# Optimization experiments

Measured on AMD Instinct MI355X. Metric: run time of the kernel, lower is better.

Reference implementation:

```python
import jax, jax.numpy as jnp
import numpy as np

B, T, C, H = 4, 2048, 1024, 16
HD = C // H  # head dim = 64

def setup_inputs() -> dict:
    key = jax.random.key(0)
    k1, k2, k3 = jax.random.split(key, 3)
    x = jax.random.normal(k1, (B, T, C), dtype=jnp.float32)
    w_attn = jax.random.normal(k2, (C, 3 * C), dtype=jnp.float32) * 0.02
    w_proj = jax.random.normal(k3, (C, C), dtype=jnp.float32) * 0.02
    return {"x": x, "w_attn": w_attn, "w_proj": w_proj}

def reference(x, w_attn, w_proj):
    b, t, c = x.shape
    qkv = x @ w_attn  # [B,T,3C]
    q, k, v = jnp.split(qkv, 3, axis=-1)
    # [B,T,C] -> [B,H,T,HD]
    def heads(z):
        return z.reshape(b, t, H, HD).transpose(0, 2, 1, 3)
    q, k, v = heads(q), heads(k), heads(v)
    scale = 1.0 / jnp.sqrt(jnp.float32(HD))
    att = jnp.einsum('bhqd,bhkd->bhqk', q, k) * scale  # [B,H,T,T]
    causal = jnp.tril(jnp.ones((t, t), dtype=bool))
    att = jnp.where(causal[None, None], att, -jnp.inf)
    att = jax.nn.softmax(att, axis=-1)
    y = jnp.einsum('bhqk,bhkd->bhqd', att, v)  # [B,H,T,HD]
    y = y.transpose(0, 2, 1, 3).reshape(b, t, c)
    return y @ w_proj
```

## Files before the change

### kernel.cpp

```cpp
#include <hip/hip_runtime.h>
#include <hip/hip_bf16.h>

typedef short bf16x8 __attribute__((ext_vector_type(8)));
typedef short short4v __attribute__((ext_vector_type(4)));
typedef float f32x4 __attribute__((ext_vector_type(4)));

template <bool V> struct BoolC { static constexpr bool value = V; };

__device__ __forceinline__ short f2b(float f) {
  __hip_bfloat16 h = __float2bfloat16(f);
  union { __hip_bfloat16 h; short s; } u; u.h = h; return u.s;
}

__device__ __forceinline__ void async_copy16(const short* g, short* l) {
  __builtin_amdgcn_global_load_lds((const __attribute__((address_space(1))) void*)g,
                                   (__attribute__((address_space(3))) void*)l, 16, 0, 0);
}

__global__ __launch_bounds__(256) void pre_kernel(const float* __restrict__ x, short* __restrict__ xb,
                                                  const float* __restrict__ wa, short* __restrict__ waT,
                                                  const float* __restrict__ wp, short* __restrict__ wpT,
                                                  float qscale) {
  const int tid = threadIdx.x;
  const int blk = blockIdx.x;
  if (blk < 8192) {
    const int i = blk * 256 + tid;
    const float4 v = ((const float4*)x)[i];
    short4v o;
    o[0] = f2b(v.x); o[1] = f2b(v.y); o[2] = f2b(v.z); o[3] = f2b(v.w);
    ((short4v*)xb)[i] = o;
    return;
  }
  __shared__ float t[32][33];
  const float* in; short* out;
  int idx, gxb, Cn, qrows; float qs;
  if (blk < 11264) { idx = blk - 8192;  in = wa; out = waT; gxb = 96; Cn = 3072; qrows = 1024; qs = qscale; }
  else             { idx = blk - 11264; in = wp; out = wpT; gxb = 32; Cn = 1024; qrows = 0;    qs = 1.0f; }
  const int bx = idx % gxb, by = idx / gxb;
  const int tx = tid & 31, ty = tid >> 5;
  const int c0 = bx * 32, r0 = by * 32;
#pragma unroll
  for (int yy = 0; yy < 32; yy += 8)
    t[ty + yy][tx] = in[(size_t)(r0 + ty + yy) * Cn + (c0 + tx)];
  __syncthreads();
#pragma unroll
  for (int yy = 0; yy < 32; yy += 8) {
    const int orow = c0 + ty + yy;
    float v = t[tx][ty + yy];
    if (orow < qrows) v *= qs;
    out[(size_t)orow * 1024 + (r0 + tx)] = f2b(v);
  }
}

__global__ __launch_bounds__(256) void vtrans_kernel(const short* __restrict__ qkv,
                                                     short* __restrict__ vT) {
  constexpr int T = 2048, C3 = 3072, HD = 64;
  const int bh = blockIdx.y, b = bh >> 4, h = bh & 15;
  const int t0 = blockIdx.x * 64;
  __shared__ short tile[64][72];
  const int tid = threadIdx.x;
  const int tr = tid >> 2, dc = (tid & 3) * 16;
  const short* src = qkv + (size_t)b * T * C3 + (size_t)(t0 + tr) * C3 + 2048 + h * HD + dc;
  *(bf16x8*)&tile[tr][dc] = *(const bf16x8*)src;
  *(bf16x8*)&tile[tr][dc + 8] = *(const bf16x8*)(src + 8);
  __syncthreads();
  const int dr = tid >> 2, tc = (tid & 3) * 16;
  bf16x8 o0, o1;
#pragma unroll
  for (int i = 0; i < 8; i++) o0[i] = tile[tc + i][dr];
#pragma unroll
  for (int i = 0; i < 8; i++) o1[i] = tile[tc + 8 + i][dr];
  short* dst = vT + ((size_t)bh * HD + dr) * T + t0 + tc;
  *(bf16x8*)dst = o0;
  *(bf16x8*)(dst + 8) = o1;
}

template <int BN, typename OutT>
__global__ __launch_bounds__(512, 2) void gemm8p_kernel(const short* __restrict__ A,
                                                        const short* __restrict__ Bt,
                                                        OutT* __restrict__ C,
                                                        int M, int N, int K) {
  constexpr int NB = BN / 64;
  constexpr int NSTREAM = NB + 4;
  __shared__ short ldsA[2][16384];
  __shared__ short ldsB[2][NB * 4096];

  const int tid = threadIdx.x;
  const int w = tid >> 6, lane = tid & 63;
  const int quad = lane >> 4, l16 = lane & 15;
  const int half = w >> 2;
  const int wn = (w & 3) * (BN / 4);
  const int wm = half * 128;

  const int gx = gridDim.x;
  const int nwg = gx * gridDim.y;
  const int flat = blockIdx.y * gx + blockIdx.x;
  const int swz = (flat & 7) * (nwg >> 3) + (flat >> 3);
  const int bn = swz % gx, bm = swz / gx;
  const int m0 = bm * 256, n0 = bn * BN;

  const int rsub = lane >> 3;
  const int cl = (lane & 7) ^ rsub;
  const short* pAsrc = A + (size_t)(m0 + half * 128 + (w & 3) * 8 + rsub) * K + cl * 8;
  const short* pBsrc = Bt + (size_t)(n0 + w * 8 + rsub) * K + cl * 8;
  const int dstoff = w * 512;

  f32x4 acc[8][NB] = {};
  bf16x8 bfr[NB][2];

  auto issue = [&](int i, int buf, int tt) {
    if (i < NB)
      async_copy16(pBsrc + (size_t)(i * 64) * K + tt * 64, &ldsB[buf][i * 4096 + dstoff]);
    else
      async_copy16(pAsrc + (size_t)((i - NB) * 32) * K + tt * 64,
                   &ldsA[buf][(i - NB) * 4096 + dstoff]);
  };

#pragma unroll
  for (int i = 0; i < NSTREAM; ++i) issue(i, 0, 0);

  const int NT = K >> 6;

#define GEMM_PHASE(P, GS, GL)                                                                  \
  {                                                                                            \
    if constexpr (LAST) { asm volatile("s_waitcnt vmcnt(" #GL ")" ::: "memory"); }             \
    else                { asm volatile("s_waitcnt vmcnt(" #GS ")" ::: "memory"); }             \
    __builtin_amdgcn_s_barrier();                                                              \
    asm volatile("" ::: "memory");                                                             \
    bf16x8 af[2][2];                                                                           \
    _Pragma("unroll") for (int mm = 0; mm < 2; ++mm)                                           \
    _Pragma("unroll") for (int kh = 0; kh < 2; ++kh)                                           \
      af[mm][kh] = *(const bf16x8*)&ldsA[buf][((P * 2 + half) * 32 + mm * 16 + l16) * 64 +     \
                                              (((kh * 4 + quad) ^ (l16 & 7)) * 8)];            \
    if constexpr (P == 0) {                                                                    \
      _Pragma("unroll") for (int nf = 0; nf < NB; ++nf)                                        \
      _Pragma("unroll") for (int kh = 0; kh < 2; ++kh)                                         \
        bfr[nf][kh] = *(const bf16x8*)&ldsB[buf][(wn + nf * 16 + l16) * 64 +                   \
                                                 (((kh * 4 + quad) ^ (l16 & 7)) * 8)];         \
    }                                                                                          \
    if constexpr (!LAST) {                                                                     \
      if constexpr (2 * P < NSTREAM) issue(2 * P, buf ^ 1, t + 1);                             \
      if constexpr (2 * P + 1 < NSTREAM) issue(2 * P + 1, buf ^ 1, t + 1);                     \
    }                                                                                          \
    __builtin_amdgcn_s_setprio(1);                                                             \
    _Pragma("unroll") for (int mm = 0; mm < 2; ++mm)                                           \
    _Pragma("unroll") for (int nf = 0; nf < NB; ++nf) {                                        \
      acc[P * 2 + mm][nf] = __builtin_amdgcn_mfma_f32_16x16x32_bf16(af[mm][0], bfr[nf][0],     \
                                                                    acc[P * 2 + mm][nf], 0, 0, 0); \
      acc[P * 2 + mm][nf] = __builtin_amdgcn_mfma_f32_16x16x32_bf16(af[mm][1], bfr[nf][1],     \
                                                                    acc[P * 2 + mm][nf], 0, 0, 0); \
    }                                                                                          \
    __builtin_amdgcn_s_setprio(0);                                                             \
    __builtin_amdgcn_s_barrier();                                                              \
  }

  auto tile = [&](int t, auto lastc) {
    constexpr bool LAST = decltype(lastc)::value;
    const int buf = t & 1;
    GEMM_PHASE(0, 3, 3)
    GEMM_PHASE(1, 4, 2)
    GEMM_PHASE(2, 5, 1)
    GEMM_PHASE(3, 6, 0)
  };

  for (int t = 0; t < NT - 1; ++t) tile(t, BoolC<false>{});
  tile(NT - 1, BoolC<true>{});
#undef GEMM_PHASE

  (void)M;
#pragma unroll
  for (int mf = 0; mf < 8; ++mf)
#pragma unroll
    for (int nf = 0; nf < NB; ++nf) {
      const int col = n0 + wn + nf * 16 + l16;
#pragma unroll
      for (int r = 0; r < 4; ++r) {
        const int row = m0 + wm + mf * 16 + quad * 4 + r;
        if constexpr (sizeof(OutT) == 4)
          C[(size_t)row * N + col] = acc[mf][nf][r];
        else
          C[(size_t)row * N + col] = f2b(acc[mf][nf][r]);
      }
    }
}

__global__ __launch_bounds__(256, 2) void attn_kernel(const short* __restrict__ qkv,
                                                      const short* __restrict__ vT,
                                                      short* __restrict__ y) {
  constexpr int T = 2048, C3 = 3072, Cc = 1024, HD = 64;
  const int bh = blockIdx.y, b = bh >> 4, h = bh & 15;
  const int tid = threadIdx.x, lane = tid & 63, wave = tid >> 6;
  const int quad = lane >> 4, l16 = lane & 15;

  __shared__ short Ksb[2][64 * 64];
  __shared__ short Vtb[2][64 * 64];
  __shared__ short Ps[4][2][16 * 68];

  const size_t base = (size_t)b * T * C3;
  const int qcol = h * HD, kcol = Cc + h * HD;
  const size_t vtbase = (size_t)bh * HD * T;

  const int r8 = lane >> 3;
  const int cg8 = ((lane & 7) ^ r8) * 8;
  const short* gk[2];
  const short* gv[2];
  short* lk[2][2]; short* lv[2][2];
#pragma unroll
  for (int t8 = 0; t8 < 2; t8++) {
    const int row = wave * 16 + t8 * 8 + r8;
    gk[t8] = qkv + base + (size_t)row * C3 + kcol + cg8;
    gv[t8] = vT + vtbase + (size_t)row * T + cg8;
#pragma unroll
    for (int bu = 0; bu < 2; bu++) {
      lk[bu][t8] = &Ksb[bu][(wave * 16 + t8 * 8) * 64];
      lv[bu][t8] = &Vtb[bu][(wave * 16 + t8 * 8) * 64];
    }
  }
  const int sw0 = ((quad) ^ (l16 & 7)) * 8;
  const int sw1 = ((quad + 4) ^ (l16 & 7)) * 8;

  bf16x8 ones;
#pragma unroll
  for (int i = 0; i < 8; i++) ones[i] = (short)0x3F80;

  for (int half = 0; half < 2; half++) {
    const int t = half ? blockIdx.x : (15 - blockIdx.x);
    const int q0 = t * 128;
    const int jmax = 2 * t + 1;

    bf16x8 qf[2][2];
#pragma unroll
    for (int s = 0; s < 2; s++) {
      const short* qp = qkv + base + (size_t)(q0 + s * 64 + wave * 16 + l16) * C3 + qcol + quad * 8;
      qf[s][0] = *(const bf16x8*)qp;
      qf[s][1] = *(const bf16x8*)(qp + 32);
    }

    f32x4 o[2][4] = {};
    f32x4 l[2] = {};

    async_copy16(gk[0], lk[0][0]);
    async_copy16(gk[1], lk[0][1]);
    async_copy16(gv[0], lv[0][0]);
    async_copy16(gv[1], lv[0][1]);

    for (int j = 0; j <= jmax; j++) {
      const int cur = j & 1;
      __syncthreads();

      if (j < jmax) {
        const size_t ko = (size_t)(j + 1) * 64 * C3;
        const int vo = (j + 1) * 64;
        async_copy16(gk[0] + ko, lk[cur ^ 1][0]);
        async_copy16(gk[1] + ko, lk[cur ^ 1][1]);
        async_copy16(gv[0] + vo, lv[cur ^ 1][0]);
        async_copy16(gv[1] + vo, lv[cur ^ 1][1]);
      }

      bf16x8 kf[4][2], vf[4][2];
#pragma unroll
      for (int nt = 0; nt < 4; nt++) {
        const int rowb = (nt * 16 + l16) * 64;
        kf[nt][0] = *(const bf16x8*)&Ksb[cur][rowb + sw0];
        kf[nt][1] = *(const bf16x8*)&Ksb[cur][rowb + sw1];
        vf[nt][0] = *(const bf16x8*)&Vtb[cur][rowb + sw0];
        vf[nt][1] = *(const bf16x8*)&Vtb[cur][rowb + sw1];
      }

      const bool lo_act = (j < jmax);

#pragma unroll
      for (int s = 0; s < 2; s++) {
        if (s == 0 && !lo_act) continue;
        f32x4 sc[4];
#pragma unroll
        for (int nt = 0; nt < 4; nt++) {
          f32x4 a = {};
          a = __builtin_amdgcn_mfma_f32_16x16x32_bf16(qf[s][0], kf[nt][0], a, 0, 0, 0);
          a = __builtin_amdgcn_mfma_f32_16x16x32_bf16(qf[s][1], kf[nt][1], a, 0, 0, 0);
          sc[nt] = a;
        }
        const bool diag = (s == 0) ? (j == jmax - 1) : (j == jmax);
        if (diag) {
#pragma unroll
          for (int nt = 0; nt < 4; nt++)
#pragma unroll
            for (int r = 0; r < 4; r++) {
              const int row_l = wave * 16 + quad * 4 + r;
              const int col_l = nt * 16 + l16;
              if (col_l > row_l) sc[nt][r] = -INFINITY;
            }
        }
#pragma unroll
        for (int nt = 0; nt < 4; nt++)
#pragma unroll
          for (int r = 0; r < 4; r++)
            Ps[wave][s][(quad * 4 + r) * 68 + nt * 16 + l16] =
                f2b(__builtin_amdgcn_exp2f(sc[nt][r]));
      }
      asm volatile("s_waitcnt lgkmcnt(0)" ::: "memory");

#pragma unroll
      for (int s = 0; s < 2; s++) {
        if (s == 0 && !lo_act) continue;
        bf16x8 pa0 = *(const bf16x8*)&Ps[wave][s][l16 * 68 + quad * 8];
        bf16x8 pa1 = *(const bf16x8*)&Ps[wave][s][l16 * 68 + 32 + quad * 8];
        f32x4 lsum = {};
        lsum = __builtin_amdgcn_mfma_f32_16x16x32_bf16(pa0, ones, lsum, 0, 0, 0);
        lsum = __builtin_amdgcn_mfma_f32_16x16x32_bf16(pa1, ones, lsum, 0, 0, 0);
        l[s] += lsum;
#pragma unroll
        for (int nt = 0; nt < 4; nt++) {
          o[s][nt] = __builtin_amdgcn_mfma_f32_16x16x32_bf16(pa0, vf[nt][0], o[s][nt], 0, 0, 0);
          o[s][nt] = __builtin_amdgcn_mfma_f32_16x16x32_bf16(pa1, vf[nt][1], o[s][nt], 0, 0, 0);
        }
      }
    }

#pragma unroll
    for (int s = 0; s < 2; s++)
#pragma unroll
      for (int nt = 0; nt < 4; nt++)
#pragma unroll
        for (int r = 0; r < 4; r++) {
          const int row_g = q0 + s * 64 + wave * 16 + quad * 4 + r;
          y[(size_t)(b * T + row_g) * Cc + h * HD + nt * 16 + l16] = f2b(o[s][nt][r] / l[s][r]);
        }
  }
}

extern "C" void kernel_launch(void* const* d_in, const int* in_sizes, int n_in,
                              void* d_out, int out_size, void* d_ws, size_t ws_size,
                              hipStream_t stream) {
  constexpr int B = 4, T = 2048, C = 1024;
  constexpr int M = B * T;
  constexpr int N1 = 3 * C;
  const float* x      = (const float*)d_in[0];
  const float* w_attn = (const float*)d_in[1];
  const float* w_proj = (const float*)d_in[2];
  float* out = (float*)d_out;

  char* ws = (char*)d_ws;
  short* xb   = (short*)(ws + 0);
  short* waT  = (short*)(ws + 16777216);
  short* wpT  = (short*)(ws + 23068672);
  short* qkvb = (short*)(ws + 25165824);
  short* yb   = (short*)(ws + 75497472);
  short* vT   = xb;

  const float qscale = 0.125f * 1.44269504088896340736f;

  pre_kernel<<<12288, 256, 0, stream>>>(x, xb, w_attn, waT, w_proj, wpT, qscale);
  gemm8p_kernel<192, short><<<dim3(N1 / 192, M / 256), 512, 0, stream>>>(xb, waT, qkvb, M, N1, C);
  vtrans_kernel<<<dim3(T / 64, B * 16), 256, 0, stream>>>(qkvb, vT);
  attn_kernel<<<dim3(8, B * 16), 256, 0, stream>>>(qkvb, vT, yb);
  gemm8p_kernel<128, float><<<dim3(C / 128, M / 256), 512, 0, stream>>>(yb, wpT, out, M, C, C);
}
```

Before: 251.1 us.

## Switch attention to 32x32 MFMA with register-resident P and remapped block order

The attention kernel moves from 16x16x32 MFMAs to 32x32x16 MFMAs, with each wave owning 32 query rows. It computes S^T so the probabilities can be repacked in registers using cvt_pk_bf16 and permlane32_swap, which removes the LDS round trip for P and its waitcnt. Waves skip key tiles past their own causal diagonal and skip the upper 32-key half when it is fully masked. The change also adds s_setprio around MFMA bursts and remaps block indices so consecutive blocks spread across heads. The risks are higher register pressure from 16-wide accumulators and extra divergence in control flow between waves.

```diff
diff --git a/kernel.cpp b/kernel.cpp
--- a/kernel.cpp
+++ b/kernel.cpp
@@ -4,12 +4,23 @@
 typedef short bf16x8 __attribute__((ext_vector_type(8)));
 typedef short short4v __attribute__((ext_vector_type(4)));
 typedef float f32x4 __attribute__((ext_vector_type(4)));
+typedef float f32x16 __attribute__((ext_vector_type(16)));
 
 template <bool V> struct BoolC { static constexpr bool value = V; };
 
 __device__ __forceinline__ short f2b(float f) {
   __hip_bfloat16 h = __float2bfloat16(f);
   union { __hip_bfloat16 h; short s; } u; u.h = h; return u.s;
+}
+
+__device__ __forceinline__ unsigned cvtpk_bf16(float lo, float hi) {
+  unsigned r;
+  asm("v_cvt_pk_bf16_f32 %0, %1, %2" : "=v"(r) : "v"(lo), "v"(hi));
+  return r;
+}
+
+__device__ __forceinline__ f32x16 mfma32(bf16x8 a, bf16x8 b, f32x16 c) {
+  return __builtin_amdgcn_mfma_f32_32x32x16_bf16(a, b, c, 0, 0, 0);
 }
 
 __device__ __forceinline__ void async_copy16(const short* g, short* l) {
@@ -188,13 +199,15 @@
                                                       const short* __restrict__ vT,
                                                       short* __restrict__ y) {
   constexpr int T = 2048, C3 = 3072, Cc = 1024, HD = 64;
-  const int bh = blockIdx.y, b = bh >> 4, h = bh & 15;
+  const int f = blockIdx.y * 8 + blockIdx.x;
+  const int bh = (f & 7) * 8 + ((f >> 3) & 7);
+  const int xb = f >> 6;
+  const int b = bh >> 4, h = bh & 15;
   const int tid = threadIdx.x, lane = tid & 63, wave = tid >> 6;
-  const int quad = lane >> 4, l16 = lane & 15;
+  const int l32 = lane & 31, hi = lane >> 5;
 
   __shared__ short Ksb[2][64 * 64];
   __shared__ short Vtb[2][64 * 64];
-  __shared__ short Ps[4][2][16 * 68];
 
   const size_t base = (size_t)b * T * C3;
   const int qcol = h * HD, kcol = Cc + h * HD;
@@ -216,28 +229,27 @@
       lv[bu][t8] = &Vtb[bu][(wave * 16 + t8 * 8) * 64];
     }
   }
-  const int sw0 = ((quad) ^ (l16 & 7)) * 8;
-  const int sw1 = ((quad + 4) ^ (l16 & 7)) * 8;
+  const int rs7 = l32 & 7;
 
   bf16x8 ones;
 #pragma unroll
   for (int i = 0; i < 8; i++) ones[i] = (short)0x3F80;
 
   for (int half = 0; half < 2; half++) {
-    const int t = half ? blockIdx.x : (15 - blockIdx.x);
+    const int t = half ? xb : (15 - xb);
     const int q0 = t * 128;
     const int jmax = 2 * t + 1;
-
-    bf16x8 qf[2][2];
-#pragma unroll
-    for (int s = 0; s < 2; s++) {
-      const short* qp = qkv + base + (size_t)(q0 + s * 64 + wave * 16 + l16) * C3 + qcol + quad * 8;
-      qf[s][0] = *(const bf16x8*)qp;
-      qf[s][1] = *(const bf16x8*)(qp + 32);
+    const int jd = 2 * t + (wave >> 1);
+    const int qrow = q0 + wave * 32 + l32;
+
+    bf16x8 qf[4];
+    {
+      const short* qp = qkv + base + (size_t)qrow * C3 + qcol + hi * 8;
+#pragma unroll
+      for (int wk = 0; wk < 4; wk++) qf[wk] = *(const bf16x8*)(qp + wk * 16);
     }
 
-    f32x4 o[2][4] = {};
-    f32x4 l[2] = {};
+    f32x16 o0 = {}, o1 = {}, lC = {};
 
     async_copy16(gk[0], lk[0][0]);
     async_copy16(gk[1], lk[0][1]);
@@ -257,75 +269,108 @@
         async_copy16(gv[1] + vo, lv[cur ^ 1][1]);
       }
 
-      bf16x8 kf[4][2], vf[4][2];
-#pragma unroll
-      for (int nt = 0; nt < 4; nt++) {
-        const int rowb = (nt * 16 + l16) * 64;
-        kf[nt][0] = *(const bf16x8*)&Ksb[cur][rowb + sw0];
-        kf[nt][1] = *(const bf16x8*)&Ksb[cur][rowb + sw1];
-        vf[nt][0] = *(const bf16x8*)&Vtb[cur][rowb + sw0];
-        vf[nt][1] = *(const bf16x8*)&Vtb[cur][rowb + sw1];
-      }
-
-      const bool lo_act = (j < jmax);
-
-#pragma unroll
-      for (int s = 0; s < 2; s++) {
-        if (s == 0 && !lo_act) continue;
-        f32x4 sc[4];
-#pragma unroll
-        for (int nt = 0; nt < 4; nt++) {
-          f32x4 a = {};
-          a = __builtin_amdgcn_mfma_f32_16x16x32_bf16(qf[s][0], kf[nt][0], a, 0, 0, 0);
-          a = __builtin_amdgcn_mfma_f32_16x16x32_bf16(qf[s][1], kf[nt][1], a, 0, 0, 0);
-          sc[nt] = a;
+      if (j > jd) continue;
+
+      const bool up = (64 * j + 32) <= (q0 + wave * 32 + 31);
+
+      f32x16 st0 = {}, st1 = {};
+      __builtin_amdgcn_s_setprio(1);
+#pragma unroll
+      for (int wk = 0; wk < 4; wk++) {
+        const bf16x8 k0 = *(const bf16x8*)&Ksb[cur][l32 * 64 + (((2 * wk + hi) ^ rs7) * 8)];
+        st0 = mfma32(k0, qf[wk], st0);
+      }
+      if (up) {
+#pragma unroll
+        for (int wk = 0; wk < 4; wk++) {
+          const bf16x8 k1 = *(const bf16x8*)&Ksb[cur][(32 + l32) * 64 + (((2 * wk + hi) ^ rs7) * 8)];
+          st1 = mfma32(k1, qf[wk], st1);
         }
-        const bool diag = (s == 0) ? (j == jmax - 1) : (j == jmax);
-        if (diag) {
-#pragma unroll
-          for (int nt = 0; nt < 4; nt++)
-#pragma unroll
-            for (int r = 0; r < 4; r++) {
-              const int row_l = wave * 16 + quad * 4 + r;
-              const int col_l = nt * 16 + l16;
-              if (col_l > row_l) sc[nt][r] = -INFINITY;
-            }
+      }
+      __builtin_amdgcn_s_setprio(0);
+
+      if (j == jd) {
+#pragma unroll
+        for (int r = 0; r < 16; r++) {
+          const int kvl = 64 * j + (r & 3) + 8 * (r >> 2) + 4 * hi;
+          if (kvl > qrow) st0[r] = -INFINITY;
+          if (up && (kvl + 32 > qrow)) st1[r] = -INFINITY;
         }
-#pragma unroll
-        for (int nt = 0; nt < 4; nt++)
-#pragma unroll
-          for (int r = 0; r < 4; r++)
-            Ps[wave][s][(quad * 4 + r) * 68 + nt * 16 + l16] =
-                f2b(__builtin_amdgcn_exp2f(sc[nt][r]));
-      }
-      asm volatile("s_waitcnt lgkmcnt(0)" ::: "memory");
-
-#pragma unroll
-      for (int s = 0; s < 2; s++) {
-        if (s == 0 && !lo_act) continue;
-        bf16x8 pa0 = *(const bf16x8*)&Ps[wave][s][l16 * 68 + quad * 8];
-        bf16x8 pa1 = *(const bf16x8*)&Ps[wave][s][l16 * 68 + 32 + quad * 8];
-        f32x4 lsum = {};
-        lsum = __builtin_amdgcn_mfma_f32_16x16x32_bf16(pa0, ones, lsum, 0, 0, 0);
-        lsum = __builtin_amdgcn_mfma_f32_16x16x32_bf16(pa1, ones, lsum, 0, 0, 0);
-        l[s] += lsum;
-#pragma unroll
-        for (int nt = 0; nt < 4; nt++) {
-          o[s][nt] = __builtin_amdgcn_mfma_f32_16x16x32_bf16(pa0, vf[nt][0], o[s][nt], 0, 0, 0);
-          o[s][nt] = __builtin_amdgcn_mfma_f32_16x16x32_bf16(pa1, vf[nt][1], o[s][nt], 0, 0, 0);
-        }
-      }
+      }
+
+      bf16x8 vf00, vf01, vf10, vf11, vf02, vf03, vf12, vf13;
+      vf00 = *(const bf16x8*)&Vtb[cur][l32 * 64 + (((0 + hi) ^ rs7) * 8)];
+      vf01 = *(const bf16x8*)&Vtb[cur][l32 * 64 + (((2 + hi) ^ rs7) * 8)];
+      vf10 = *(const bf16x8*)&Vtb[cur][(32 + l32) * 64 + (((0 + hi) ^ rs7) * 8)];
+      vf11 = *(const bf16x8*)&Vtb[cur][(32 + l32) * 64 + (((2 + hi) ^ rs7) * 8)];
+      if (up) {
+        vf02 = *(const bf16x8*)&Vtb[cur][l32 * 64 + (((4 + hi) ^ rs7) * 8)];
+        vf03 = *(const bf16x8*)&Vtb[cur][l32 * 64 + (((6 + hi) ^ rs7) * 8)];
+        vf12 = *(const bf16x8*)&Vtb[cur][(32 + l32) * 64 + (((4 + hi) ^ rs7) * 8)];
+        vf13 = *(const bf16x8*)&Vtb[cur][(32 + l32) * 64 + (((6 + hi) ^ rs7) * 8)];
+      }
+
+#pragma unroll
+      for (int r = 0; r < 16; r++) st0[r] = __builtin_amdgcn_exp2f(st0[r]);
+      bf16x8 pa0, pa1, pa2, pa3;
+      {
+        unsigned a0 = cvtpk_bf16(st0[0], st0[1]), c0 = cvtpk_bf16(st0[2], st0[3]);
+        unsigned b0 = cvtpk_bf16(st0[4], st0[5]), d0 = cvtpk_bf16(st0[6], st0[7]);
+        asm volatile("v_permlane32_swap_b32 %0, %1" : "+v"(a0), "+v"(b0));
+        asm volatile("v_permlane32_swap_b32 %0, %1" : "+v"(c0), "+v"(d0));
+        union { unsigned u[4]; bf16x8 v; } p; p.u[0] = a0; p.u[1] = c0; p.u[2] = b0; p.u[3] = d0;
+        pa0 = p.v;
+        unsigned a1 = cvtpk_bf16(st0[8], st0[9]), c1 = cvtpk_bf16(st0[10], st0[11]);
+        unsigned b1 = cvtpk_bf16(st0[12], st0[13]), d1 = cvtpk_bf16(st0[14], st0[15]);
+        asm volatile("v_permlane32_swap_b32 %0, %1" : "+v"(a1), "+v"(b1));
+        asm volatile("v_permlane32_swap_b32 %0, %1" : "+v"(c1), "+v"(d1));
+        union { unsigned u[4]; bf16x8 v; } q; q.u[0] = a1; q.u[1] = c1; q.u[2] = b1; q.u[3] = d1;
+        pa1 = q.v;
+      }
+      if (up) {
+#pragma unroll
+        for (int r = 0; r < 16; r++) st1[r] = __builtin_amdgcn_exp2f(st1[r]);
+        unsigned a2 = cvtpk_bf16(st1[0], st1[1]), c2 = cvtpk_bf16(st1[2], st1[3]);
+        unsigned b2 = cvtpk_bf16(st1[4], st1[5]), d2 = cvtpk_bf16(st1[6], st1[7]);
+        asm volatile("v_permlane32_swap_b32 %0, %1" : "+v"(a2), "+v"(b2));
+        asm volatile("v_permlane32_swap_b32 %0, %1" : "+v"(c2), "+v"(d2));
+        union { unsigned u[4]; bf16x8 v; } p; p.u[0] = a2; p.u[1] = c2; p.u[2] = b2; p.u[3] = d2;
+        pa2 = p.v;
+        unsigned a3 = cvtpk_bf16(st1[8], st1[9]), c3 = cvtpk_bf16(st1[10], st1[11]);
+        unsigned b3 = cvtpk_bf16(st1[12], st1[13]), d3 = cvtpk_bf16(st1[14], st1[15]);
+        asm volatile("v_permlane32_swap_b32 %0, %1" : "+v"(a3), "+v"(b3));
+        asm volatile("v_permlane32_swap_b32 %0, %1" : "+v"(c3), "+v"(d3));
+        union { unsigned u[4]; bf16x8 v; } q; q.u[0] = a3; q.u[1] = c3; q.u[2] = b3; q.u[3] = d3;
+        pa3 = q.v;
+      }
+
+      __builtin_amdgcn_s_setprio(1);
+      lC = mfma32(pa0, ones, lC);
+      lC = mfma32(pa1, ones, lC);
+      o0 = mfma32(pa0, vf00, o0);
+      o0 = mfma32(pa1, vf01, o0);
+      o1 = mfma32(pa0, vf10, o1);
+      o1 = mfma32(pa1, vf11, o1);
+      if (up) {
+        lC = mfma32(pa2, ones, lC);
+        lC = mfma32(pa3, ones, lC);
+        o0 = mfma32(pa2, vf02, o0);
+        o0 = mfma32(pa3, vf03, o0);
+        o1 = mfma32(pa2, vf12, o1);
+        o1 = mfma32(pa3, vf13, o1);
+      }
+      __builtin_amdgcn_s_setprio(0);
     }
 
 #pragma unroll
-    for (int s = 0; s < 2; s++)
-#pragma unroll
-      for (int nt = 0; nt < 4; nt++)
-#pragma unroll
-        for (int r = 0; r < 4; r++) {
-          const int row_g = q0 + s * 64 + wave * 16 + quad * 4 + r;
-          y[(size_t)(b * T + row_g) * Cc + h * HD + nt * 16 + l16] = f2b(o[s][nt][r] / l[s][r]);
-        }
+    for (int r = 0; r < 16; r++) {
+      const int rq = (r & 3) + 8 * (r >> 2) + 4 * hi;
+      const int row_g = q0 + wave * 32 + rq;
+      const float inv = 1.0f / lC[r];
+      short* yp = y + (size_t)(b * T + row_g) * Cc + h * HD;
+      yp[l32] = f2b(o0[r] * inv);
+      yp[32 + l32] = f2b(o1[r] * inv);
+    }
   }
 }
 
```

After: 229.2 us. -8.7%, faster.
